# Performance work log

Hardware: AMD Instinct MI355X
Metric: run time of the kernel (lower is better)

Reference implementation:

```python
import jax, jax.numpy as jnp
import numpy as np

# Static problem sizes (must match input construction)
B, G, EPG, K, C = 64, 24, 512, 20, 1
NS = B * G            # total number of subgraphs
E = NS * EPG          # total number of edges
M, H = 4096, 256      # node_state shape


def setup_inputs() -> dict:
    key = jax.random.key(0)
    ks = jax.random.split(key, 8)
    label = (jax.random.uniform(ks[0], (E,)) < 0.5).astype(jnp.float32)
    label0 = (jax.random.uniform(ks[1], (E,)) < 0.5).astype(jnp.float32)
    log_theta = jax.random.normal(ks[2], (E, K), dtype=jnp.float32)
    log_theta0 = jax.random.normal(ks[3], (E, K), dtype=jnp.float32)
    log_alpha = jax.random.normal(ks[4], (E, K), dtype=jnp.float32)
    log_alpha0 = jax.random.normal(ks[5], (E, K), dtype=jnp.float32)
    subgraph_idx = (jnp.arange(E, dtype=jnp.int32) // EPG).astype(jnp.int32)
    subgraph_idx0 = subgraph_idx
    subgraph_idx_base = (jnp.arange(B + 1, dtype=jnp.int32) * (G * C)).astype(jnp.int32)
    subgraph_idx_base0 = subgraph_idx_base
    node_state = jax.random.normal(ks[6], (M, H), dtype=jnp.float32)
    node_state0 = jax.random.normal(ks[7], (M, H), dtype=jnp.float32)
    return {
        "label": label, "label0": label0,
        "log_theta": log_theta, "log_theta0": log_theta0,
        "log_alpha": log_alpha, "log_alpha0": log_alpha0,
        "subgraph_idx": subgraph_idx, "subgraph_idx0": subgraph_idx0,
        "subgraph_idx_base": subgraph_idx_base, "subgraph_idx_base0": subgraph_idx_base0,
        "node_state": node_state, "node_state0": node_state0,
    }


def _bce_with_logits(logits, y):
    # BCEWithLogitsLoss(reduction='none'), broadcast label over K mixture components
    return -(y[:, None] * jax.nn.log_sigmoid(logits)
             + (1.0 - y)[:, None] * jax.nn.log_sigmoid(-logits))


def _stream_loss(label, log_theta, log_alpha, subgraph_idx, subgraph_idx_base):
    adj_loss = _bce_with_logits(log_theta, label)                     # E x K
    const = jax.ops.segment_sum(jnp.ones((E,), jnp.float32), subgraph_idx, NS)  # edges per subgraph
    reduce_adj_loss = jax.ops.segment_sum(adj_loss, subgraph_idx, NS)  # NS x K
    reduce_log_alpha = jax.ops.segment_sum(log_alpha, subgraph_idx, NS) / const[:, None]
    reduce_log_alpha = jax.nn.log_softmax(reduce_log_alpha, axis=-1)
    log_prob = jax.nn.logsumexp(-reduce_adj_loss + reduce_log_alpha, axis=1)  # NS
    # bc_idx: map each subgraph to its (batch, canonical-order) slot; C == 1 here,
    # equivalent to repeat_interleave(arange(B*C), bc_size) in the original.
    bc_idx = jnp.searchsorted(subgraph_idx_base, jnp.arange(NS, dtype=jnp.int32), side='right') - 1
    bc_log_prob = jax.ops.segment_sum(log_prob, bc_idx, B * C).reshape(B, C)
    bc_const = jax.ops.segment_sum(const, bc_idx, B * C).reshape(B, C)
    bc_loss = bc_log_prob / bc_const
    b_loss = jax.nn.logsumexp(bc_loss, axis=1)   # sum_order_log_prob=False
    return jnp.mean(-b_loss)                      # reduction='mean'


def _trace_cdist(ns, ns0):
    # Fused replacement for the naive O(m^2) host-side pairwise-distance loop:
    # D[i,j] = ||ns[i] - ns0[j]||, then trace(D).
    x2 = jnp.sum(ns * ns, axis=1)
    y2 = jnp.sum(ns0 * ns0, axis=1)
    d2 = x2[:, None] + y2[None, :] - 2.0 * (ns @ ns0.T)   # M x M
    D = jnp.sqrt(jnp.maximum(d2, 0.0))
    return jnp.trace(D)


def reference(label, label0, log_theta, log_theta0, log_alpha, log_alpha0,
              subgraph_idx, subgraph_idx0, subgraph_idx_base, subgraph_idx_base0,
              node_state, node_state0):
    loss = _stream_loss(label, log_theta, log_alpha, subgraph_idx, subgraph_idx_base)
    loss0 = _stream_loss(label0, log_theta0, log_alpha0, subgraph_idx0, subgraph_idx_base0)
    trD = _trace_cdist(node_state, node_state0)
    # return_neg_log_prob=False branch of the original
    return 10.0 * (loss + loss0) + trD
```

## Files before the change

kernel.cpp:

```cpp
#include <hip/hip_runtime.h>
#include <math.h>

#define B_   64
#define G_   24
#define EPG_ 512
#define K_   20
#define NS_  (B_ * G_)
#define E_   (NS_ * EPG_)
#define M_   4096
#define H_   256

__global__ __launch_bounds__(320)
void stream_loss_kernel(const float* __restrict__ label,
                        const float* __restrict__ label0,
                        const float* __restrict__ log_theta,
                        const float* __restrict__ log_theta0,
                        const float* __restrict__ log_alpha,
                        const float* __restrict__ log_alpha0,
                        float* __restrict__ out)
{
    const int s   = blockIdx.x;
    const int tid = threadIdx.x;

    const float* lab = (blockIdx.y == 0) ? label     : label0;
    const float* lt  = (blockIdx.y == 0) ? log_theta : log_theta0;
    const float* la  = (blockIdx.y == 0) ? log_alpha : log_alpha0;

    __shared__ float s_label[EPG_];
    __shared__ float red_adj[320];
    __shared__ float red_alpha[320];
    __shared__ float S_adj[K_];
    __shared__ float S_alpha[K_];

    const float* labp = lab + (size_t)s * EPG_;
    for (int i = tid; i < EPG_; i += 320) s_label[i] = labp[i];
    __syncthreads();

    const int e_l = tid / K_;

    float acc_adj = 0.0f, acc_alpha = 0.0f;
    const size_t base = (size_t)s * EPG_ * K_;
    for (int e0 = 0; e0 < EPG_; e0 += 16) {
        const float  y   = s_label[e0 + e_l];
        const size_t idx = base + (size_t)e0 * K_ + tid;
        const float  x   = lt[idx];
        const float adj = fmaxf(x, 0.0f) - x * y + log1pf(__expf(-fabsf(x)));
        acc_adj   += adj;
        acc_alpha += la[idx];
    }
    red_adj[tid]   = acc_adj;
    red_alpha[tid] = acc_alpha;
    __syncthreads();

    if (tid < K_) {
        float sa = 0.0f, sl = 0.0f;
        #pragma unroll
        for (int g = 0; g < 16; ++g) {
            sa += red_adj[g * K_ + tid];
            sl += red_alpha[g * K_ + tid];
        }
        S_adj[tid]   = sa;
        S_alpha[tid] = sl;
    }
    __syncthreads();

    if (tid == 0) {
        const float inv_const = 1.0f / (float)EPG_;
        float m1 = -INFINITY;
        #pragma unroll
        for (int i = 0; i < K_; ++i) m1 = fmaxf(m1, S_alpha[i] * inv_const);
        float sum1 = 0.0f;
        #pragma unroll
        for (int i = 0; i < K_; ++i) sum1 += __expf(S_alpha[i] * inv_const - m1);
        const float lse = m1 + __logf(sum1);

        float m2 = -INFINITY;
        #pragma unroll
        for (int i = 0; i < K_; ++i) {
            const float v = -S_adj[i] + S_alpha[i] * inv_const - lse;
            m2 = fmaxf(m2, v);
        }
        float sum2 = 0.0f;
        #pragma unroll
        for (int i = 0; i < K_; ++i) {
            const float v = -S_adj[i] + S_alpha[i] * inv_const - lse;
            sum2 += __expf(v - m2);
        }
        const float lp = m2 + __logf(sum2);

        atomicAdd(out, lp * (-10.0f / (float)E_));
    }
}

__global__ __launch_bounds__(256)
void trace_cdist_kernel(const float* __restrict__ ns,
                        const float* __restrict__ ns0,
                        float* __restrict__ out)
{
    const int wave = threadIdx.x >> 6;
    const int lane = threadIdx.x & 63;
    __shared__ float s_d[16];

    #pragma unroll
    for (int i = 0; i < 4; ++i) {
        const int row = blockIdx.x * 16 + wave * 4 + i;
        const float4* a = (const float4*)(ns  + (size_t)row * H_);
        const float4* b = (const float4*)(ns0 + (size_t)row * H_);
        const float4 av = a[lane];
        const float4 bv = b[lane];
        const float dx = av.x - bv.x;
        const float dy = av.y - bv.y;
        const float dz = av.z - bv.z;
        const float dw = av.w - bv.w;
        float sv = dx * dx + dy * dy + dz * dz + dw * dw;
        #pragma unroll
        for (int off = 32; off > 0; off >>= 1) sv += __shfl_down(sv, off);
        if (lane == 0) s_d[wave * 4 + i] = sqrtf(sv);
    }
    __syncthreads();
    if (threadIdx.x == 0) {
        float t = 0.0f;
        #pragma unroll
        for (int i = 0; i < 16; ++i) t += s_d[i];
        atomicAdd(out, t);
    }
}

extern "C" void kernel_launch(void* const* d_in, const int* in_sizes, int n_in,
                              void* d_out, int out_size, void* d_ws, size_t ws_size,
                              hipStream_t stream) {
    const float* label       = (const float*)d_in[0];
    const float* label0      = (const float*)d_in[1];
    const float* log_theta   = (const float*)d_in[2];
    const float* log_theta0  = (const float*)d_in[3];
    const float* log_alpha   = (const float*)d_in[4];
    const float* log_alpha0  = (const float*)d_in[5];
    const float* node_state  = (const float*)d_in[10];
    const float* node_state0 = (const float*)d_in[11];
    float* out = (float*)d_out;

    hipMemsetAsync(out, 0, sizeof(float), stream);

    dim3 grid(NS_, 2);
    stream_loss_kernel<<<grid, 320, 0, stream>>>(label, label0,
                                                 log_theta, log_theta0,
                                                 log_alpha, log_alpha0, out);
    trace_cdist_kernel<<<M_ / 16, 256, 0, stream>>>(node_state, node_state0, out);
}
```

Before: 299.3 us.

## Split stream loss into flat float4 partial-sum kernel plus per-subgraph finalize

Replaces the one-block-per-subgraph loop with a flat grid where each thread loads one float4 of log_theta and log_alpha, accumulates per-component partials with shared-memory atomics, and adds them into per-subgraph workspace bins with global atomics. A separate finalize kernel then computes the log-softmax and logsumexp per subgraph. The aim is more memory-level parallelism and vectorized loads for the bandwidth-bound pass. The cost is heavy shared-atomic contention on only 40 bins, plus global atomics, an extra memset and an extra kernel launch.

After: 498.6 us. 66.6% more time.

```diff
diff --git a/kernel.cpp b/kernel.cpp
--- a/kernel.cpp
+++ b/kernel.cpp
@@ -10,86 +10,86 @@
 #define M_   4096
 #define H_   256
 
-__global__ __launch_bounds__(320)
-void stream_loss_kernel(const float* __restrict__ label,
+#define F4S_ (E_ * K_ / 4)
+#define BLK1 256
+#define NB1  (F4S_ / BLK1)
+#define SGF4 (EPG_ * K_ / 4)
+#define BPS  (SGF4 / BLK1)
+
+__global__ __launch_bounds__(BLK1)
+void bce_partial_kernel(const float* __restrict__ label,
                         const float* __restrict__ label0,
                         const float* __restrict__ log_theta,
                         const float* __restrict__ log_theta0,
                         const float* __restrict__ log_alpha,
                         const float* __restrict__ log_alpha0,
-                        float* __restrict__ out)
+                        float* __restrict__ ws)
 {
-    const int s   = blockIdx.x;
-    const int tid = threadIdx.x;
+    const int t  = threadIdx.x;
+    const int b  = blockIdx.x;
+    const int st = blockIdx.y;
 
-    const float* lab = (blockIdx.y == 0) ? label     : label0;
-    const float* lt  = (blockIdx.y == 0) ? log_theta : log_theta0;
-    const float* la  = (blockIdx.y == 0) ? log_alpha : log_alpha0;
+    const float*  lab = st ? label0     : label;
+    const float4* lt4 = (const float4*)(st ? log_theta0 : log_theta);
+    const float4* la4 = (const float4*)(st ? log_alpha0 : log_alpha);
 
-    __shared__ float s_label[EPG_];
-    __shared__ float red_adj[320];
-    __shared__ float red_alpha[320];
-    __shared__ float S_adj[K_];
-    __shared__ float S_alpha[K_];
+    const int f4 = b * BLK1 + t;
+    const float  y = lab[f4 / 5];
+    const float4 x = lt4[f4];
+    const float4 a = la4[f4];
 
-    const float* labp = lab + (size_t)s * EPG_;
-    for (int i = tid; i < EPG_; i += 320) s_label[i] = labp[i];
+    __shared__ float bins[2 * K_];
+    if (t < 2 * K_) bins[t] = 0.0f;
     __syncthreads();
 
-    const int e_l = tid / K_;
-
-    float acc_adj = 0.0f, acc_alpha = 0.0f;
-    const size_t base = (size_t)s * EPG_ * K_;
-    for (int e0 = 0; e0 < EPG_; e0 += 16) {
-        const float  y   = s_label[e0 + e_l];
-        const size_t idx = base + (size_t)e0 * K_ + tid;
-        const float  x   = lt[idx];
-        const float adj = fmaxf(x, 0.0f) - x * y + log1pf(__expf(-fabsf(x)));
-        acc_adj   += adj;
-        acc_alpha += la[idx];
-    }
-    red_adj[tid]   = acc_adj;
-    red_alpha[tid] = acc_alpha;
+    const int kb = 4 * (f4 % 5);
+    atomicAdd(&bins[kb + 0], fmaxf(x.x, 0.f) - x.x * y + __logf(1.f + __expf(-fabsf(x.x))));
+    atomicAdd(&bins[kb + 1], fmaxf(x.y, 0.f) - x.y * y + __logf(1.f + __expf(-fabsf(x.y))));
+    atomicAdd(&bins[kb + 2], fmaxf(x.z, 0.f) - x.z * y + __logf(1.f + __expf(-fabsf(x.z))));
+    atomicAdd(&bins[kb + 3], fmaxf(x.w, 0.f) - x.w * y + __logf(1.f + __expf(-fabsf(x.w))));
+    atomicAdd(&bins[K_ + kb + 0], a.x);
+    atomicAdd(&bins[K_ + kb + 1], a.y);
+    atomicAdd(&bins[K_ + kb + 2], a.z);
+    atomicAdd(&bins[K_ + kb + 3], a.w);
     __syncthreads();
 
-    if (tid < K_) {
-        float sa = 0.0f, sl = 0.0f;
-        #pragma unroll
-        for (int g = 0; g < 16; ++g) {
-            sa += red_adj[g * K_ + tid];
-            sl += red_alpha[g * K_ + tid];
-        }
-        S_adj[tid]   = sa;
-        S_alpha[tid] = sl;
+    if (t < 2 * K_) {
+        const int s = b / BPS;
+        atomicAdd(&ws[(size_t)(st * NS_ + s) * (2 * K_) + t], bins[t]);
     }
-    __syncthreads();
+}
 
-    if (tid == 0) {
-        const float inv_const = 1.0f / (float)EPG_;
-        float m1 = -INFINITY;
-        #pragma unroll
-        for (int i = 0; i < K_; ++i) m1 = fmaxf(m1, S_alpha[i] * inv_const);
-        float sum1 = 0.0f;
-        #pragma unroll
-        for (int i = 0; i < K_; ++i) sum1 += __expf(S_alpha[i] * inv_const - m1);
-        const float lse = m1 + __logf(sum1);
+__global__ __launch_bounds__(256)
+void finalize_kernel(const float* __restrict__ ws, float* __restrict__ out)
+{
+    const int i = blockIdx.x * 256 + threadIdx.x;
+    if (i >= 2 * NS_) return;
+    const float* p = ws + (size_t)i * (2 * K_);
 
-        float m2 = -INFINITY;
-        #pragma unroll
-        for (int i = 0; i < K_; ++i) {
-            const float v = -S_adj[i] + S_alpha[i] * inv_const - lse;
-            m2 = fmaxf(m2, v);
-        }
-        float sum2 = 0.0f;
-        #pragma unroll
-        for (int i = 0; i < K_; ++i) {
-            const float v = -S_adj[i] + S_alpha[i] * inv_const - lse;
-            sum2 += __expf(v - m2);
-        }
-        const float lp = m2 + __logf(sum2);
+    const float inv_const = 1.0f / (float)EPG_;
+    float m1 = -INFINITY;
+    #pragma unroll
+    for (int k = 0; k < K_; ++k) m1 = fmaxf(m1, p[K_ + k] * inv_const);
+    float sum1 = 0.0f;
+    #pragma unroll
+    for (int k = 0; k < K_; ++k) sum1 += __expf(p[K_ + k] * inv_const - m1);
+    const float lse = m1 + __logf(sum1);
 
-        atomicAdd(out, lp * (-10.0f / (float)E_));
+    float m2 = -INFINITY;
+    #pragma unroll
+    for (int k = 0; k < K_; ++k) {
+        const float v = -p[k] + p[K_ + k] * inv_const - lse;
+        m2 = fmaxf(m2, v);
     }
+    float sum2 = 0.0f;
+    #pragma unroll
+    for (int k = 0; k < K_; ++k) {
+        const float v = -p[k] + p[K_ + k] * inv_const - lse;
+        sum2 += __expf(v - m2);
+    }
+    const float lp = m2 + __logf(sum2);
+
+    atomicAdd(out, lp * (-10.0f / (float)E_));
 }
 
 __global__ __launch_bounds__(256)
@@ -138,12 +138,15 @@
     const float* node_state  = (const float*)d_in[10];
     const float* node_state0 = (const float*)d_in[11];
     float* out = (float*)d_out;
+    float* ws  = (float*)d_ws;
 
     hipMemsetAsync(out, 0, sizeof(float), stream);
+    hipMemsetAsync(ws, 0, (size_t)(2 * NS_) * (2 * K_) * sizeof(float), stream);
 
-    dim3 grid(NS_, 2);
-    stream_loss_kernel<<<grid, 320, 0, stream>>>(label, label0,
-                                                 log_theta, log_theta0,
-                                                 log_alpha, log_alpha0, out);
+    dim3 grid1(NB1, 2);
+    bce_partial_kernel<<<grid1, BLK1, 0, stream>>>(label, label0,
+                                                   log_theta, log_theta0,
+                                                   log_alpha, log_alpha0, ws);
+    finalize_kernel<<<(2 * NS_ + 255) / 256, 256, 0, stream>>>(ws, out);
     trace_cdist_kernel<<<M_ / 16, 256, 0, stream>>>(node_state, node_state0, out);
 }
```
